# Kernel tuning notes

Measured on AMD Instinct MI355X. Metric: run time of the kernel, lower is better.

The kernel has to match this reference:

```python
import jax, jax.numpy as jnp
import numpy as np

NHEAD = 16  # n_head; head_size N = C // NHEAD = 64


def _forward(x, time_maa_x, time_maa, time_maa_w1, time_maa_w2,
             time_decay, time_decay_w1, time_decay_w2,
             time_aaaaa, time_aaa_w1, time_aaa_w2,
             time_kkk_w1, time_kkk_w2,
             gate_w1, gate_w2,
             time_misc_a, ma_w1, ma_w2,
             time_misc_k, mk_w1, mk_w2,
             receptance, key_w, value, output,
             ln_w, ln_b, time_faaaa):
    B, T, C = x.shape
    H, N = NHEAD, C // NHEAD
    # --- fused_time_shift: token shift + 4-way LoRA mixing (rg, wa, k, v) ---
    xprev = jnp.pad(x, ((0, 0), (1, 0), (0, 0)))[:, :T]   # shift right by one token
    xx = xprev - x
    xxx = x + xx * time_maa_x
    mix = jnp.tanh(xxx @ time_maa_w1.T).reshape(B, T, 4, -1)        # (B,T,4,32)
    deltas = jnp.einsum('btfd,fcd->fbtc', mix, time_maa_w2)         # (4,B,T,C)
    xrg, xwa, xk, xv = x[None] + xx[None] * (time_maa + deltas)
    # --- projections + small LoRAs ---
    r = xrg @ receptance.T
    g = jnp.tanh(xrg @ gate_w1.T) @ gate_w2.T                       # gate
    k = xk @ key_w.T
    kk1 = jnp.tanh(xk @ time_kkk_w1.T)
    mk1 = xk @ mk_w1.T
    v = xv @ value.T
    w1 = jnp.tanh(xwa @ time_decay_w1.T)
    a1 = xwa @ time_aaa_w1.T
    ma1 = xwa @ ma_w1.T
    # data-dependent log-decay, clamped <= -0.5 via softplus
    w = -jax.nn.softplus(-(time_decay + w1 @ time_decay_w2.T)) - 0.5
    # removal key kk: per-head L2-normalized
    kk = k + kk1 @ time_kkk_w2.T
    kk = kk.reshape(B, T, H, N)
    kk = kk / jnp.maximum(jnp.linalg.norm(kk, axis=-1, keepdims=True), 1e-12)
    kk = kk.reshape(B, T, C)
    a = jax.nn.sigmoid(time_aaaaa + a1 @ time_aaa_w2.T)
    ma = jax.nn.sigmoid(time_misc_a + ma1 @ ma_w2.T)
    k = k * ma + k * a * (1 - ma)
    mk = jax.nn.sigmoid(time_misc_k + mk1 @ mk_w2.T)
    k = k * jnp.exp(w * mk)
    b = -kk * a
    # --- RWKV-7 linear-attention scan; state S: (B,H,N_value,N_key) ---
    def heads(z):
        return z.reshape(B, T, H, N).transpose(1, 0, 2, 3)          # (T,B,H,N)
    rh, wh, kh, vh, kkh, bh = map(heads, (r, w, k, v, kk, b))

    def step(S, inp):
        r_, w_, k_, v_, kk_, b_ = inp
        sab = jnp.einsum('bhvk,bhk->bhv', S, kk_)                   # S @ kk
        S = (S * jnp.exp(w_)[:, :, None, :]                         # diag decay on key dim
             + sab[..., None] * b_[:, :, None, :]                   # (S kk) b^T  (delta-rule removal)
             + v_[..., None] * k_[:, :, None, :])                   # v k^T
        y = jnp.einsum('bhvk,bhk->bhv', S, r_)
        return S, y

    S0 = jnp.zeros((B, H, N, N), x.dtype)
    _, y = jax.lax.scan(step, S0, (rh, wh, kh, vh, kkh, bh))
    y = y.transpose(1, 0, 2, 3)                                     # (B,T,H,N)
    # --- GroupNorm (H groups, eps=64e-5) + r.k bonus + gate (fused_attn_ln tail) ---
    mu = y.mean(-1, keepdims=True)
    var = ((y - mu) ** 2).mean(-1, keepdims=True)
    yn = (y - mu) / jnp.sqrt(var + 0.00064) * ln_w.reshape(H, N) + ln_b.reshape(H, N)
    r4 = r.reshape(B, T, H, N)
    k4 = k.reshape(B, T, H, N)
    v4 = v.reshape(B, T, H, N)
    bonus = (r4 * k4 * time_faaaa.reshape(H, N)).sum(-1, keepdims=True) * v4
    out = (yn + bonus).reshape(B, T, C) * g
    return out @ output.T


def setup_inputs() -> dict:
    key = jax.random.key(0)
    ks = iter(jax.random.split(key, 40))
    B, T, C = 2, 1024, 1024
    def n(shape, s=1.0):
        return jax.random.normal(next(ks), shape, jnp.float32) * s
    def u(shape, lo, hi):
        return jax.random.uniform(next(ks), shape, jnp.float32, lo, hi)
    d = {}
    d['x'] = n((B, T, C))
    d['time_maa_x'] = u((1, 1, C), 0.0, 1.0)
    d['time_maa'] = u((4, 1, 1, C), 0.0, 1.0)
    d['time_maa_w1'] = n((128, C), 0.02)
    d['time_maa_w2'] = n((4, C, 32), 0.05)
    d['time_decay'] = u((1, 1, C), -6.5, -1.5)
    d['time_decay_w1'] = n((64, C), 0.02)
    d['time_decay_w2'] = n((C, 64), 0.05)
    d['time_aaaaa'] = n((1, 1, C), 0.1)
    d['time_aaa_w1'] = n((16, C), 0.02)
    d['time_aaa_w2'] = n((C, 16), 0.05)
    d['time_kkk_w1'] = n((16, C), 0.02)
    d['time_kkk_w2'] = n((C, 16), 0.05)
    d['gate_w1'] = n((128, C), 0.05)
    d['gate_w2'] = n((C, 128), 0.05)
    d['time_misc_a'] = n((1, 1, C), 0.1)
    d['ma_w1'] = n((16, C), 0.02)
    d['ma_w2'] = n((C, 16), 0.05)
    d['time_misc_k'] = n((1, 1, C), 0.1)
    d['mk_w1'] = n((16, C), 0.02)
    d['mk_w2'] = n((C, 16), 0.05)
    s = 0.5 / C ** 0.5
    d['receptance'] = u((C, C), -s, s)
    d['key_w'] = u((C, C), -0.1 * s, 0.1 * s)
    d['value'] = u((C, C), -s, s)
    d['output'] = n((C, C), 0.02)
    d['ln_w'] = jnp.ones((C,), jnp.float32)
    d['ln_b'] = jnp.zeros((C,), jnp.float32)
    d['time_faaaa'] = n((C,), 0.1)
    return d


def reference(x, time_maa_x, time_maa, time_maa_w1, time_maa_w2,
              time_decay, time_decay_w1, time_decay_w2,
              time_aaaaa, time_aaa_w1, time_aaa_w2,
              time_kkk_w1, time_kkk_w2,
              gate_w1, gate_w2,
              time_misc_a, ma_w1, ma_w2,
              time_misc_k, mk_w1, mk_w2,
              receptance, key_w, value, output,
              ln_w, ln_b, time_faaaa):
    return _forward(x, time_maa_x, time_maa, time_maa_w1, time_maa_w2,
                    time_decay, time_decay_w1, time_decay_w2,
                    time_aaaaa, time_aaa_w1, time_aaa_w2,
                    time_kkk_w1, time_kkk_w2,
                    gate_w1, gate_w2,
                    time_misc_a, ma_w1, ma_w2,
                    time_misc_k, mk_w1, mk_w2,
                    receptance, key_w, value, output,
                    ln_w, ln_b, time_faaaa)
```

## Files before the change

kernel.cpp:

```cpp
#include <hip/hip_runtime.h>
#include <hip/hip_bf16.h>

typedef __hip_bfloat16 bf16;

#define B_ 2
#define T_ 1024
#define C_ 1024
#define H_ 16
#define N_ 64

using short4v = __attribute__((ext_vector_type(4))) short;
using short8 = __attribute__((ext_vector_type(8))) short;
using f32x4 = __attribute__((ext_vector_type(4))) float;

__device__ __forceinline__ float bs2f(short s) {
  return __uint_as_float(((unsigned int)(unsigned short)s) << 16);
}
__device__ __forceinline__ bf16 f2bf(float f) { return __float2bfloat16(f); }
__device__ __forceinline__ short bfbits(float f) {
  bf16 h = __float2bfloat16(f);
  return *reinterpret_cast<short*>(&h);
}
__device__ __forceinline__ float sigmoidf_(float x) { return 1.0f / (1.0f + expf(-x)); }
__device__ __forceinline__ float softplusf_(float x) {
  return fmaxf(x, 0.0f) + log1pf(expf(-fabsf(x)));
}
__device__ __forceinline__ float qsum16(float x) {
  int a = __builtin_amdgcn_update_dpp(0, __float_as_int(x), 0xB1, 0xF, 0xF, true);
  x += __int_as_float(a);
  int b = __builtin_amdgcn_update_dpp(0, __float_as_int(x), 0x4E, 0xF, 0xF, true);
  x += __int_as_float(b);
  int c = __builtin_amdgcn_update_dpp(0, __float_as_int(x), 0x124, 0xF, 0xF, true);
  x += __int_as_float(c);
  int d = __builtin_amdgcn_update_dpp(0, __float_as_int(x), 0x128, 0xF, 0xF, true);
  x += __int_as_float(d);
  return x;
}
__device__ __forceinline__ void qsum16x2(float& x, float& y) {
  int a0 = __builtin_amdgcn_update_dpp(0, __float_as_int(x), 0xB1, 0xF, 0xF, true);
  int b0 = __builtin_amdgcn_update_dpp(0, __float_as_int(y), 0xB1, 0xF, 0xF, true);
  x += __int_as_float(a0); y += __int_as_float(b0);
  int a1 = __builtin_amdgcn_update_dpp(0, __float_as_int(x), 0x4E, 0xF, 0xF, true);
  int b1 = __builtin_amdgcn_update_dpp(0, __float_as_int(y), 0x4E, 0xF, 0xF, true);
  x += __int_as_float(a1); y += __int_as_float(b1);
  int a2 = __builtin_amdgcn_update_dpp(0, __float_as_int(x), 0x124, 0xF, 0xF, true);
  int b2 = __builtin_amdgcn_update_dpp(0, __float_as_int(y), 0x124, 0xF, 0xF, true);
  x += __int_as_float(a2); y += __int_as_float(b2);
  int a3 = __builtin_amdgcn_update_dpp(0, __float_as_int(x), 0x128, 0xF, 0xF, true);
  int b3 = __builtin_amdgcn_update_dpp(0, __float_as_int(y), 0x128, 0xF, 0xF, true);
  x += __int_as_float(a3); y += __int_as_float(b3);
}

__global__ __launch_bounds__(256) void cvt_all_kernel(
    const float* __restrict__ s0, const float* __restrict__ s1,
    const float* __restrict__ s2, const float* __restrict__ s3,
    const float* __restrict__ s4, const float* __restrict__ s5,
    const float* __restrict__ s6,
    bf16* __restrict__ d0, bf16* __restrict__ d1, bf16* __restrict__ d2w,
    bf16* __restrict__ d3, bf16* __restrict__ d4, bf16* __restrict__ d5,
    bf16* __restrict__ d6,
    const float* __restrict__ tkw1, const float* __restrict__ mkw1,
    const float* __restrict__ tdw1, const float* __restrict__ taw1,
    const float* __restrict__ maw1,
    bf16* __restrict__ wsk, bf16* __restrict__ wswa,
    const float* __restrict__ tmw2, const float* __restrict__ tdw2,
    const float* __restrict__ tkw2, const float* __restrict__ taw2,
    const float* __restrict__ maw2, const float* __restrict__ mkw2,
    bf16* __restrict__ tmw2e, bf16* __restrict__ w2e5) {
  long bidx = blockIdx.x;
  const float* s; bf16* d; long off;
  if (bidx < 4480) {
    long i4 = bidx * 256 + threadIdx.x;
    if (i4 < 32768) { s = s0; d = d0; off = i4; }
    else if (i4 < 294912) { s = s1; d = d1; off = i4 - 32768; }
    else if (i4 < 327680) { s = s2; d = d2w; off = i4 - 294912; }
    else if (i4 < 360448) { s = s3; d = d3; off = i4 - 327680; }
    else if (i4 < 622592) { s = s4; d = d4; off = i4 - 360448; }
    else if (i4 < 884736) { s = s5; d = d5; off = i4 - 622592; }
    else { s = s6; d = d6; off = i4 - 884736; }
  } else if (bidx < 4608) {
    long i4 = (bidx - 4480) * 256 + threadIdx.x;
    long so, dof;
    if (i4 < 4096) { s = tkw1; so = i4; d = wsk; dof = i4; }
    else if (i4 < 8192) { s = mkw1; so = i4 - 4096; d = wsk; dof = i4; }
    else if (i4 < 24576) { s = tdw1; so = i4 - 8192; d = wswa; dof = i4 - 8192; }
    else if (i4 < 28672) { s = taw1; so = i4 - 24576; d = wswa; dof = i4 - 8192; }
    else { s = maw1; so = i4 - 28672; d = wswa; dof = i4 - 8192; }
    float4 v = *(const float4*)(s + so * 4);
    d[dof * 4 + 0] = f2bf(v.x); d[dof * 4 + 1] = f2bf(v.y);
    d[dof * 4 + 2] = f2bf(v.z); d[dof * 4 + 3] = f2bf(v.w);
    return;
  } else if (bidx < 5120) {
    long i4 = (bidx - 4608) * 256 + threadIdx.x;
    long n = i4 >> 5;
    int k0 = (int)(i4 & 31) << 2;
    int f = (int)(n >> 10);
    float4 v = {0.f, 0.f, 0.f, 0.f};
    if ((k0 >> 5) == f) v = *(const float4*)(tmw2 + n * 32 + (k0 & 31));
    tmw2e[i4 * 4 + 0] = f2bf(v.x);
    tmw2e[i4 * 4 + 1] = f2bf(v.y);
    tmw2e[i4 * 4 + 2] = f2bf(v.z);
    tmw2e[i4 * 4 + 3] = f2bf(v.w);
    return;
  } else {
    long i4 = (bidx - 5120) * 256 + threadIdx.x;
    long rowi = i4 >> 5;
    int k0 = (int)(i4 & 31) << 2;
    int j = (int)(rowi >> 10);
    int c = (int)(rowi & 1023);
    float4 v = {0.f, 0.f, 0.f, 0.f};
    if (j == 0) { if (k0 < 64) v = *(const float4*)(tdw2 + c * 64 + k0); }
    else if (j == 1) { if (k0 >= 64 && k0 < 80) v = *(const float4*)(taw2 + c * 16 + (k0 - 64)); }
    else if (j == 2) { if (k0 >= 80 && k0 < 96) v = *(const float4*)(maw2 + c * 16 + (k0 - 80)); }
    else if (j == 3) { if (k0 >= 96 && k0 < 112) v = *(const float4*)(tkw2 + c * 16 + (k0 - 96)); }
    else { if (k0 >= 112) v = *(const float4*)(mkw2 + c * 16 + (k0 - 112)); }
    w2e5[i4 * 4 + 0] = f2bf(v.x);
    w2e5[i4 * 4 + 1] = f2bf(v.y);
    w2e5[i4 * 4 + 2] = f2bf(v.z);
    w2e5[i4 * 4 + 3] = f2bf(v.w);
    return;
  }
  float4 v = *(const float4*)(s + off * 4);
// ... 24 lines not shown
  float* Cf = gb.Cf[z];
  bf16* Cb = gb.Cb[z];
  int tid = threadIdx.x;
  int arow = tid >> 1, acol = (tid & 1) << 5;
  int wrow = tid >> 2, wcol = (tid & 3) << 4;
  int wv = tid >> 6, lane = tid & 63;
  int fr = lane & 15, fq = lane >> 4;
  bool wok = (n0 + wrow) < Nz;
  const bf16* Ap = A + (long)(m0 + arow) * K + acol;
  const bf16* Wp = W + (long)(n0 + wrow) * K + wcol;
  short8 zz = {0, 0, 0, 0, 0, 0, 0, 0};
  f32x4 a00 = {0.f, 0.f, 0.f, 0.f};
  f32x4 a01 = a00, a02 = a00, a03 = a00, a10 = a00, a11 = a00, a12 = a00, a13 = a00;
  for (int k0 = 0; k0 < K; k0 += 64) {
    *(short8*)&As[arow][acol] = *(const short8*)(Ap + k0);
    *(short8*)&As[arow][acol + 8] = *(const short8*)(Ap + k0 + 8);
    *(short8*)&As[arow][acol + 16] = *(const short8*)(Ap + k0 + 16);
    *(short8*)&As[arow][acol + 24] = *(const short8*)(Ap + k0 + 24);
    *(short8*)&Ws[wrow][wcol] = wok ? *(const short8*)(Wp + k0) : zz;
    *(short8*)&Ws[wrow][wcol + 8] = wok ? *(const short8*)(Wp + k0 + 8) : zz;
    __syncthreads();
#pragma unroll
    for (int kk = 0; kk < 2; kk++) {
      int ko = (fq << 3) + (kk << 5);
      short8 af0 = *(const short8*)&As[(wv << 5) + fr][ko];
      short8 af1 = *(const short8*)&As[(wv << 5) + 16 + fr][ko];
      short8 b0 = *(const short8*)&Ws[fr][ko];
      short8 b1 = *(const short8*)&Ws[16 + fr][ko];
      short8 b2 = *(const short8*)&Ws[32 + fr][ko];
      short8 b3 = *(const short8*)&Ws[48 + fr][ko];
      a00 = __builtin_amdgcn_mfma_f32_16x16x32_bf16(af0, b0, a00, 0, 0, 0);
      a01 = __builtin_amdgcn_mfma_f32_16x16x32_bf16(af0, b1, a01, 0, 0, 0);
      a02 = __builtin_amdgcn_mfma_f32_16x16x32_bf16(af0, b2, a02, 0, 0, 0);
      a03 = __builtin_amdgcn_mfma_f32_16x16x32_bf16(af0, b3, a03, 0, 0, 0);
      a10 = __builtin_amdgcn_mfma_f32_16x16x32_bf16(af1, b0, a10, 0, 0, 0);
      a11 = __builtin_amdgcn_mfma_f32_16x16x32_bf16(af1, b1, a11, 0, 0, 0);
      a12 = __builtin_amdgcn_mfma_f32_16x16x32_bf16(af1, b2, a12, 0, 0, 0);
      a13 = __builtin_amdgcn_mfma_f32_16x16x32_bf16(af1, b3, a13, 0, 0, 0);
    }
    __syncthreads();
  }
  int ocol = n0 + fr;
  int orow0 = m0 + (wv << 5) + (fq << 2);
#define WRB(accv, mf, nt) { int col = ocol + ((nt) << 4); if (col < Nz) { \
    _Pragma("unroll") for (int r = 0; r < 4; r++) { \
      float vvv = accv[r]; if (col < actN) vvv = tanhf(vvv); \
      long oi = (long)(orow0 + ((mf) << 4) + r) * ldc + coff + col; \
      if (Cb) Cb[oi] = f2bf(vvv); else Cf[oi] = vvv; } } }
  WRB(a00, 0, 0) WRB(a01, 0, 1) WRB(a02, 0, 2) WRB(a03, 0, 3)
  WRB(a10, 1, 0) WRB(a11, 1, 1) WRB(a12, 1, 2) WRB(a13, 1, 3)
#undef WRB
}

__global__ __launch_bounds__(256) void gemm_mix_kernel(
    const float* __restrict__ x, const float* __restrict__ tmx,
    const bf16* __restrict__ W, bf16* __restrict__ Cb) {
  __shared__ __align__(16) bf16 As[128][72];
  __shared__ __align__(16) bf16 Ws[64][72];
  const int K = 1024;
  int n0 = blockIdx.x << 6;
  int m0 = blockIdx.y << 7;
  int tid = threadIdx.x;
  int arow = tid >> 1, acol = (tid & 1) << 5;
  int wrow = tid >> 2, wcol = (tid & 3) << 4;
  int wv = tid >> 6, lane = tid & 63;
  int fr = lane & 15, fq = lane >> 4;
  int grow = m0 + arow;
  int t = grow & (T_ - 1);
  const float* xp = x + (long)grow * C_ + acol;
  const bf16* Wp = W + (long)(n0 + wrow) * K + wcol;
  f32x4 a00 = {0.f, 0.f, 0.f, 0.f};
  f32x4 a01 = a00, a02 = a00, a03 = a00, a10 = a00, a11 = a00, a12 = a00, a13 = a00;
  for (int k0 = 0; k0 < K; k0 += 64) {
#pragma unroll
    for (int jj = 0; jj < 4; jj++) {
      int co = k0 + (jj << 3);
      float4 c0 = *(const float4*)(xp + co);
      float4 c1 = *(const float4*)(xp + co + 4);
      float4 q0 = {0.f, 0.f, 0.f, 0.f}, q1 = q0;
      if (t > 0) {
        q0 = *(const float4*)(xp + co - C_);
        q1 = *(const float4*)(xp + co + 4 - C_);
      }
      float4 m0v = *(const float4*)(tmx + co + acol);
      float4 m1v = *(const float4*)(tmx + co + acol + 4);
      short8 sv;
      sv[0] = bfbits(fmaf(q0.x - c0.x, m0v.x, c0.x));
      sv[1] = bfbits(fmaf(q0.y - c0.y, m0v.y, c0.y));
      sv[2] = bfbits(fmaf(q0.z - c0.z, m0v.z, c0.z));
      sv[3] = bfbits(fmaf(q0.w - c0.w, m0v.w, c0.w));
      sv[4] = bfbits(fmaf(q1.x - c1.x, m1v.x, c1.x));
      sv[5] = bfbits(fmaf(q1.y - c1.y, m1v.y, c1.y));
      sv[6] = bfbits(fmaf(q1.z - c1.z, m1v.z, c1.z));
      sv[7] = bfbits(fmaf(q1.w - c1.w, m1v.w, c1.w));
      *(short8*)&As[arow][acol + (jj << 3)] = sv;
    }
    *(short8*)&Ws[wrow][wcol] = *(const short8*)(Wp + k0);
    *(short8*)&Ws[wrow][wcol + 8] = *(const short8*)(Wp + k0 + 8);
    __syncthreads();
#pragma unroll
    for (int kk = 0; kk < 2; kk++) {
      int ko = (fq << 3) + (kk << 5);
      short8 af0 = *(const short8*)&As[(wv << 5) + fr][ko];
      short8 af1 = *(const short8*)&As[(wv << 5) + 16 + fr][ko];
      short8 b0 = *(const short8*)&Ws[fr][ko];
      short8 b1 = *(const short8*)&Ws[16 + fr][ko];
      short8 b2 = *(const short8*)&Ws[32 + fr][ko];
      short8 b3 = *(const short8*)&Ws[48 + fr][ko];
      a00 = __builtin_amdgcn_mfma_f32_16x16x32_bf16(af0, b0, a00, 0, 0, 0);
      a01 = __builtin_amdgcn_mfma_f32_16x16x32_bf16(af0, b1, a01, 0, 0, 0);
      a02 = __builtin_amdgcn_mfma_f32_16x16x32_bf16(af0, b2, a02, 0, 0, 0);
      a03 = __builtin_amdgcn_mfma_f32_16x16x32_bf16(af0, b3, a03, 0, 0, 0);
      a10 = __builtin_amdgcn_mfma_f32_16x16x32_bf16(af1, b0, a10, 0, 0, 0);
      a11 = __builtin_amdgcn_mfma_f32_16x16x32_bf16(af1, b1, a11, 0, 0, 0);
      a12 = __builtin_amdgcn_mfma_f32_16x16x32_bf16(af1, b2, a12, 0, 0, 0);
      a13 = __builtin_amdgcn_mfma_f32_16x16x32_bf16(af1, b3, a13, 0, 0, 0);
    }
    __syncthreads();
  }
  const int Nz = 128;
  int ocol = n0 + fr;
  int orow0 = m0 + (wv << 5) + (fq << 2);
#define WRM(accv, mf, nt) { int col = ocol + ((nt) << 4); \
    _Pragma("unroll") for (int r = 0; r < 4; r++) { \
      long oi = (long)(orow0 + ((mf) << 4) + r) * Nz + col; \
      Cb[oi] = f2bf(tanhf(accv[r])); } }
  WRM(a00, 0, 0) WRM(a01, 0, 1) WRM(a02, 0, 2) WRM(a03, 0, 3)
  WRM(a10, 1, 0) WRM(a11, 1, 1) WRM(a12, 1, 2) WRM(a13, 1, 3)
#undef WRM
}

__global__ __launch_bounds__(256) void gemm_mixapply_kernel(
    const bf16* __restrict__ A, const bf16* __restrict__ W,
    const float* __restrict__ x, const float* __restrict__ tmaa,
    bf16* __restrict__ xrg, bf16* __restrict__ xwa,
    bf16* __restrict__ xk, bf16* __restrict__ xv) {
  __shared__ __align__(16) bf16 As[128][72];
  __shared__ __align__(16) bf16 Ws[64][72];
  const int K = 128;
  int n0 = blockIdx.x << 6;
  int m0 = blockIdx.y << 7;
  int tid = threadIdx.x;
  int arow = tid >> 1, acol = (tid & 1) << 5;
  int wrow = tid >> 2, wcol = (tid & 3) << 4;
  int wv = tid >> 6, lane = tid & 63;
  int fr = lane & 15, fq = lane >> 4;
  const bf16* Ap = A + (long)(m0 + arow) * K + acol;
  const bf16* Wp = W + (long)(n0 + wrow) * K + wcol;
  f32x4 a00 = {0.f, 0.f, 0.f, 0.f};
  f32x4 a01 = a00, a02 = a00, a03 = a00, a10 = a00, a11 = a00, a12 = a00, a13 = a00;
  for (int k0 = 0; k0 < K; k0 += 64) {
    *(short8*)&As[arow][acol] = *(const short8*)(Ap + k0);
    *(short8*)&As[arow][acol + 8] = *(const short8*)(Ap + k0 + 8);
    *(short8*)&As[arow][acol + 16] = *(const short8*)(Ap + k0 + 16);
    *(short8*)&As[arow][acol + 24] = *(const short8*)(Ap + k0 + 24);
    *(short8*)&Ws[wrow][wcol] = *(const short8*)(Wp + k0);
    *(short8*)&Ws[wrow][wcol + 8] = *(const short8*)(Wp + k0 + 8);
    __syncthreads();
#pragma unroll
    for (int kk = 0; kk < 2; kk++) {
      int ko = (fq << 3) + (kk << 5);
      short8 af0 = *(const short8*)&As[(wv << 5) + fr][ko];
      short8 af1 = *(const short8*)&As[(wv << 5) + 16 + fr][ko];
      short8 b0 = *(const short8*)&Ws[fr][ko];
      short8 b1 = *(const short8*)&Ws[16 + fr][ko];
      short8 b2 = *(const short8*)&Ws[32 + fr][ko];
      short8 b3 = *(const short8*)&Ws[48 + fr][ko];
      a00 = __builtin_amdgcn_mfma_f32_16x16x32_bf16(af0, b0, a00, 0, 0, 0);
      a01 = __builtin_amdgcn_mfma_f32_16x16x32_bf16(af0, b1, a01, 0, 0, 0);
      a02 = __builtin_amdgcn_mfma_f32_16x16x32_bf16(af0, b2, a02, 0, 0, 0);
      a03 = __builtin_amdgcn_mfma_f32_16x16x32_bf16(af0, b3, a03, 0, 0, 0);
      a10 = __builtin_amdgcn_mfma_f32_16x16x32_bf16(af1, b0, a10, 0, 0, 0);
      a11 = __builtin_amdgcn_mfma_f32_16x16x32_bf16(af1, b1, a11, 0, 0, 0);
      a12 = __builtin_amdgcn_mfma_f32_16x16x32_bf16(af1, b2, a12, 0, 0, 0);
      a13 = __builtin_amdgcn_mfma_f32_16x16x32_bf16(af1, b3, a13, 0, 0, 0);
    }
    __syncthreads();
  }
  int f = n0 >> 10;
  int c0 = n0 & 1023;
  bf16* outp = (f == 0) ? xrg : (f == 1) ? xwa : (f == 2) ? xk : xv;
  int ocol = c0 + fr;
  int orow0 = m0 + (wv << 5) + (fq << 2);
#define WRA(accv, mf, nt) { int cc = ocol + ((nt) << 4); \
    float ta = tmaa[(f << 10) + cc]; \
    _Pragma("unroll") for (int r = 0; r < 4; r++) { \
      int row = orow0 + ((mf) << 4) + r; \
      int t = row & (T_ - 1); \
      long xo = (long)row * C_ + cc; \
      float xb = x[xo]; \
      float xq = (t > 0) ? x[xo - C_] : 0.0f; \
      outp[xo] = f2bf(fmaf(xq - xb, ta + accv[r], xb)); } }
  WRA(a00, 0, 0) WRA(a01, 0, 1) WRA(a02, 0, 2) WRA(a03, 0, 3)
  WRA(a10, 1, 0) WRA(a11, 1, 1) WRA(a12, 1, 2) WRA(a13, 1, 3)
#undef WRA
}

__global__ __launch_bounds__(256) void fuse2_kernel(
    const float* __restrict__ kraw, const float* __restrict__ d2,
    const float* __restrict__ tdec, const float* __restrict__ taa,
    const float* __restrict__ tma, const float* __restrict__ tmk,
    float* __restrict__ ew, float* __restrict__ kfin,
    float* __restrict__ kkn, float* __restrict__ bbo) {
  int m = blockIdx.x, tid = threadIdx.x;
  int c4 = tid << 2;
  const float* dp = d2 + (long)m * 5120;
  float4 wd4 = *(const float4*)(dp + c4);
  float4 ad4 = *(const float4*)(dp + 1024 + c4);
  float4 mad4 = *(const float4*)(dp + 2048 + c4);
  float4 kd4 = *(const float4*)(dp + 3072 + c4);
  float4 mkd4 = *(const float4*)(dp + 4096 + c4);
  float4 kraw4 = *(const float4*)(kraw + (long)m * C_ + c4);
  float4 tdec4 = *(const float4*)(tdec + c4);
  float4 taa4 = *(const float4*)(taa + c4);
  float4 tma4 = *(const float4*)(tma + c4);
  float4 tmk4 = *(const float4*)(tmk + c4);
  float wd[4] = {wd4.x, wd4.y, wd4.z, wd4.w};
  float ad[4] = {ad4.x, ad4.y, ad4.z, ad4.w};
  float mad[4] = {mad4.x, mad4.y, mad4.z, mad4.w};
  float kd[4] = {kd4.x, kd4.y, kd4.z, kd4.w};
  float mkd[4] = {mkd4.x, mkd4.y, mkd4.z, mkd4.w};
  float krw[4] = {kraw4.x, kraw4.y, kraw4.z, kraw4.w};
  float td[4] = {tdec4.x, tdec4.y, tdec4.z, tdec4.w};
  float ta[4] = {taa4.x, taa4.y, taa4.z, taa4.w};
  float tm[4] = {tma4.x, tma4.y, tma4.z, tma4.w};
  float tk[4] = {tmk4.x, tmk4.y, tmk4.z, tmk4.w};
  float kkp[4], av[4], wvv[4], kr[4], mkv[4];
  float sumsq = 0.f;
#pragma unroll
  for (int j = 0; j < 4; j++) {
    float w = -softplusf_(-(td[j] + wd[j])) - 0.5f;
    wvv[j] = w;
    float kkpre = krw[j] + kd[j];
    kkp[j] = kkpre;
    sumsq += kkpre * kkpre;
    float a = sigmoidf_(ta[j] + ad[j]);
    av[j] = a;
    float ma = sigmoidf_(tm[j] + mad[j]);
    float mk = sigmoidf_(tk[j] + mkd[j]);
    mkv[j] = mk;
    kr[j] = krw[j] * (ma + a * (1.f - ma));
  }
  sumsq += __shfl_xor(sumsq, 1);
  sumsq += __shfl_xor(sumsq, 2);
  sumsq += __shfl_xor(sumsq, 4);
  sumsq += __shfl_xor(sumsq, 8);
  float rn = 1.0f / fmaxf(sqrtf(sumsq), 1e-12f);
  float4 kknv, bbov, eww, kfv;
  float* kknp = (float*)&kknv;
  float* bbop = (float*)&bbov;
  float* ewp = (float*)&eww;
  float* kfp = (float*)&kfv;
#pragma unroll
  for (int j = 0; j < 4; j++) {
    float kkx = kkp[j] * rn;
    kknp[j] = kkx;
    bbop[j] = -kkx * av[j];
    ewp[j] = expf(wvv[j]);
    kfp[j] = kr[j] * expf(wvv[j] * mkv[j]);
  }
  long off4 = (long)m * C_ + c4;
  *(float4*)(kkn + off4) = kknv;
  *(float4*)(bbo + off4) = bbov;
  *(float4*)(ew + off4) = eww;
  *(float4*)(kfin + off4) = kfv;
}

#define SCHUNK 16
#define NCHUNK (T_ / SCHUNK)
__global__ __launch_bounds__(256, 1) void scan_kernel(
    const float* __restrict__ rB, const float* __restrict__ ewB,
    const float* __restrict__ kB, const float* __restrict__ vB,
    const float* __restrict__ kkB, const float* __restrict__ bbB,
    float* __restrict__ yB) {
  __shared__ __align__(16) float lds[2][6][SCHUNK * 64];
  int bid = blockIdx.x;
  int bh = bid >> 2, rg = bid & 3;
  int b = bh >> 4, h = bh & 15;
  int tid = threadIdx.x;
  int wave = tid >> 6, lane = tid & 63;
  int g = lane >> 4, q = lane & 15;
  int row = (rg << 4) + (wave << 2) + g;
  int kq = q << 2;
  const long base = ((long)b * T_) * C_ + (h << 6);
  const float* s0 = kkB + base;
  const float* s1 = ewB + base;
  const float* s2 = kB + base;
  const float* s3 = bbB + base;
  const float* s4 = rB + base;
  const float* s5 = vB + base;
  int stok = tid >> 4;
  int spc = (tid & 15) << 2;
  int lo = (stok << 6) + spc;
  float4 rb0, rb1, rb2, rb3, rb4, rb5;
  auto loadc = [&](int c) {
    long go = (long)((c << 4) + stok) * C_ + spc;
    rb0 = *(const float4*)(s0 + go);
    rb1 = *(const float4*)(s1 + go);
    rb2 = *(const float4*)(s2 + go);
    rb3 = *(const float4*)(s3 + go);
    rb4 = *(const float4*)(s4 + go);
    rb5 = *(const float4*)(s5 + go);
  };
  auto stage = [&](int buf) {
    *(float4*)&lds[buf][0][lo] = rb0;
    *(float4*)&lds[buf][1][lo] = rb1;
    *(float4*)&lds[buf][2][lo] = rb2;
    *(float4*)&lds[buf][3][lo] = rb3;
    *(float4*)&lds[buf][4][lo] = rb4;
    *(float4*)&lds[buf][5][lo] = rb5;
  };
  float S0 = 0.f, S1 = 0.f, S2 = 0.f, S3 = 0.f;
  float ypv = 0.f;
  float4 Q0kk, Q0ew, Q0k, Q0bb, Q0r; float Q0v;
  float4 Q1kk, Q1ew, Q1k, Q1bb, Q1r; float Q1v;
  float4 Q2kk, Q2ew, Q2k, Q2bb, Q2r; float Q2v;

#define PF(i, tt) { int tb_ = ((tt) << 6); \
    Q##i##kk = *(const float4*)&lds[cur][0][tb_ + kq]; \
    Q##i##ew = *(const float4*)&lds[cur][1][tb_ + kq]; \
    Q##i##k  = *(const float4*)&lds[cur][2][tb_ + kq]; \
    Q##i##bb = *(const float4*)&lds[cur][3][tb_ + kq]; \
    Q##i##r  = *(const float4*)&lds[cur][4][tb_ + kq]; \
    Q##i##v  = lds[cur][5][tb_ + row]; }
#define SBAR __builtin_amdgcn_sched_barrier(0x7)
#define ST(i, gtok, FIRSTT) { \
    float p_ = fmaf(S1, Q##i##kk.y, S0 * Q##i##kk.x) + \
               fmaf(S3, Q##i##kk.w, S2 * Q##i##kk.z); \
    float yo_ = ypv; \
    qsum16x2(p_, yo_); \
    if (q == 0 && !((FIRSTT) && c == 0)) \
      yB[base + (long)((gtok) - 1) * C_ + row] = yo_; \
    float n0 = fmaf(S0, Q##i##ew.x, Q##i##v * Q##i##k.x); \
    float n1 = fmaf(S1, Q##i##ew.y, Q##i##v * Q##i##k.y); \
    float n2 = fmaf(S2, Q##i##ew.z, Q##i##v * Q##i##k.z); \
    float n3 = fmaf(S3, Q##i##ew.w, Q##i##v * Q##i##k.w); \
    S0 = fmaf(p_, Q##i##bb.x, n0); \
    S1 = fmaf(p_, Q##i##bb.y, n1); \
    S2 = fmaf(p_, Q##i##bb.z, n2); \
    S3 = fmaf(p_, Q##i##bb.w, n3); \
    ypv = fmaf(S1, Q##i##r.y, S0 * Q##i##r.x) + \
          fmaf(S3, Q##i##r.w, S2 * Q##i##r.z); }

  loadc(0);
  stage(0);
  loadc(1);
  __syncthreads();
  int cur = 0;
  for (int c = 0; c < NCHUNK; c++) {
    int t0 = c << 4;
    PF(0, 0); PF(1, 1);
    if (c + 1 < NCHUNK) stage(cur ^ 1);
    if (c + 2 < NCHUNK) loadc(c + 2);
    SBAR;
    PF(2, 2);  SBAR; ST(0, t0 + 0, true);
    PF(0, 3);  SBAR; ST(1, t0 + 1, false);
    PF(1, 4);  SBAR; ST(2, t0 + 2, false);
    PF(2, 5);  SBAR; ST(0, t0 + 3, false);
    PF(0, 6);  SBAR; ST(1, t0 + 4, false);
    PF(1, 7);  SBAR; ST(2, t0 + 5, false);
    PF(2, 8);  SBAR; ST(0, t0 + 6, false);
    PF(0, 9);  SBAR; ST(1, t0 + 7, false);
    PF(1, 10); SBAR; ST(2, t0 + 8, false);
    PF(2, 11); SBAR; ST(0, t0 + 9, false);
    PF(0, 12); SBAR; ST(1, t0 + 10, false);
    PF(1, 13); SBAR; ST(2, t0 + 11, false);
    PF(2, 14); SBAR; ST(0, t0 + 12, false);
    PF(0, 15); SBAR; ST(1, t0 + 13, false);
    ST(2, t0 + 14, false);
    ST(0, t0 + 15, false);
    __syncthreads();
    cur ^= 1;
  }
  {
    float yo = qsum16(ypv);
    if (q == 0) yB[base + (long)(T_ - 1) * C_ + row] = yo;
  }
#undef PF
#undef SBAR
#undef ST
}

__global__ __launch_bounds__(256) void gnout_kernel(
    const float* __restrict__ y, const float* __restrict__ r,
    const float* __restrict__ kf, const float* __restrict__ v,
    const float* __restrict__ g,
    const float* __restrict__ lnw, const float* __restrict__ lnb,
    const float* __restrict__ fa, bf16* __restrict__ z) {
  int tid = threadIdx.x;
  int w = tid >> 6, lane = tid & 63;
  int gi = (blockIdx.x << 2) + w;
  int h = gi & 15, mt = gi >> 4;
  long off = (long)mt * C_ + (h << 6) + lane;
  float yv = y[off];
  float s = yv;
  s += __shfl_xor(s, 1); s += __shfl_xor(s, 2); s += __shfl_xor(s, 4);
  s += __shfl_xor(s, 8); s += __shfl_xor(s, 16); s += __shfl_xor(s, 32);
  float mu = s * (1.0f / 64.0f);
  float d = yv - mu;
  float s2 = d * d;
  s2 += __shfl_xor(s2, 1); s2 += __shfl_xor(s2, 2); s2 += __shfl_xor(s2, 4);
  s2 += __shfl_xor(s2, 8); s2 += __shfl_xor(s2, 16); s2 += __shfl_xor(s2, 32);
  float var = s2 * (1.0f / 64.0f);
  int hc = (h << 6) + lane;
  float dot = r[off] * kf[off] * fa[hc];
  dot += __shfl_xor(dot, 1); dot += __shfl_xor(dot, 2); dot += __shfl_xor(dot, 4);
  dot += __shfl_xor(dot, 8); dot += __shfl_xor(dot, 16); dot += __shfl_xor(dot, 32);
  float yn = d * rsqrtf(var + 0.00064f) * lnw[hc] + lnb[hc];
  z[off] = f2bf((yn + dot * v[off]) * g[off]);
}

extern "C" void kernel_launch(void* const* d_in, const int* in_sizes, int n_in,
                              void* d_out, int out_size, void* d_ws, size_t ws_size,
                              hipStream_t stream) {
  const float* x = (const float*)d_in[0];
  const float* tmx = (const float*)d_in[1];
  const float* tmaa = (const float*)d_in[2];
  const float* tmw1 = (const float*)d_in[3];
  const float* tmw2 = (const float*)d_in[4];
  const float* tdec = (const float*)d_in[5];
  const float* tdw1 = (const float*)d_in[6];
  const float* tdw2 = (const float*)d_in[7];
  const float* taa5 = (const float*)d_in[8];
  const float* taw1 = (const float*)d_in[9];
  const float* taw2 = (const float*)d_in[10];
  const float* tkw1 = (const float*)d_in[11];
  const float* tkw2 = (const float*)d_in[12];
  const float* gw1 = (const float*)d_in[13];
  const float* gw2 = (const float*)d_in[14];
  const float* tmia = (const float*)d_in[15];
  const float* maw1 = (const float*)d_in[16];
  const float* maw2 = (const float*)d_in[17];
  const float* tmik = (const float*)d_in[18];
  const float* mkw1 = (const float*)d_in[19];
  const float* mkw2 = (const float*)d_in[20];
  const float* wrec = (const float*)d_in[21];
  const float* wkey = (const float*)d_in[22];
  const float* wval = (const float*)d_in[23];
  const float* wout = (const float*)d_in[24];
  const float* lnw = (const float*)d_in[25];
  const float* lnb = (const float*)d_in[26];
  const float* faaa = (const float*)d_in[27];

  const long MT = 2048, CC = 1024;
  char* base = (char*)d_ws;
  float* y = (float*)base;     base += MT * CC * 4;
  bf16* xrgb = (bf16*)base;    base += MT * CC * 2;
  bf16* xwab = (bf16*)base;    base += MT * CC * 2;
  bf16* xkb = (bf16*)base;     base += MT * CC * 2;
  bf16* xvb = (bf16*)base;     base += MT * CC * 2;
  float* rr = (float*)base;    base += MT * CC * 4;
  float* kraw = (float*)base;  base += MT * CC * 4;
  float* vv = (float*)base;    base += MT * CC * 4;
  float* gg = (float*)base;    base += MT * CC * 4;
  float* bbo = (float*)base;   base += MT * CC * 4;
  bf16* g1b = (bf16*)base;     base += MT * 128 * 2;
  bf16* out12b = (bf16*)base;  base += MT * 128 * 2;
  bf16* zb = (bf16*)base;      base += MT * CC * 2;
  bf16* mixb = (bf16*)base;    base += MT * 128 * 2;
  float* d2 = (float*)base;    base += MT * 5120L * 4;
  bf16* tmw1b = (bf16*)base;   base += 128 * CC * 2;
  bf16* wrecb = (bf16*)base;   base += CC * CC * 2;
  bf16* gw1b = (bf16*)base;    base += 128 * CC * 2;
  bf16* gw2b = (bf16*)base;    base += CC * 128 * 2;
  bf16* wkeyb = (bf16*)base;   base += CC * CC * 2;
  bf16* wvalb = (bf16*)base;   base += CC * CC * 2;
  bf16* woutb = (bf16*)base;   base += CC * CC * 2;
  bf16* wskb = (bf16*)base;    base += 32 * CC * 2;
  bf16* wswab = (bf16*)base;   base += 96 * CC * 2;
  bf16* tmw2e = (bf16*)base;   base += 4096L * 128 * 2;
  bf16* w2e5b = (bf16*)base;   base += 5120L * 128 * 2;
  float* ew = kraw;
  float* kfin = (float*)xrgb;
  float* kkn = (float*)xkb;

  cvt_all_kernel<<<5760, 256, 0, stream>>>(
      tmw1, wrec, gw1, gw2, wkey, wval, wout,
      tmw1b, wrecb, gw1b, gw2b, wkeyb, wvalb, woutb,
      tkw1, mkw1, tdw1, taw1, maw1, wskb, wswab,
      tmw2, tdw2, tkw2, taw2, maw2, mkw2,
      tmw2e, w2e5b);

  gemm_mix_kernel<<<dim3(2, 16), 256, 0, stream>>>(x, tmx, tmw1b, mixb);
  gemm_mixapply_kernel<<<dim3(64, 16), 256, 0, stream>>>(
      mixb, tmw2e, x, tmaa, xrgb, xwab, xkb, xvb);
  {
    GemmBatch gb = {};
    gb.A[0] = xrgb; gb.W[0] = wrecb; gb.Cf[0] = rr;      gb.Cb[0] = nullptr; gb.N[0] = 1024; gb.actN[0] = 0;   gb.ldc[0] = 1024; gb.coff[0] = 0;
    gb.A[1] = xrgb; gb.W[1] = gw1b;  gb.Cf[1] = nullptr; gb.Cb[1] = g1b;     gb.N[1] = 128;  gb.actN[1] = 128; gb.ldc[1] = 128;  gb.coff[1] = 0;
    gb.A[2] = xkb;  gb.W[2] = wkeyb; gb.Cf[2] = kraw;    gb.Cb[2] = nullptr; gb.N[2] = 1024; gb.actN[2] = 0;   gb.ldc[2] = 1024; gb.coff[2] = 0;
    gb.A[3] = xkb;  gb.W[3] = wskb;  gb.Cf[3] = nullptr; gb.Cb[3] = out12b;  gb.N[3] = 32;   gb.actN[3] = 16;  gb.ldc[3] = 128;  gb.coff[3] = 96;
    gb.A[4] = xvb;  gb.W[4] = wvalb; gb.Cf[4] = vv;      gb.Cb[4] = nullptr; gb.N[4] = 1024; gb.actN[4] = 0;   gb.ldc[4] = 1024; gb.coff[4] = 0;
    gb.A[5] = xwab; gb.W[5] = wswab; gb.Cf[5] = nullptr; gb.Cb[5] = out12b;  gb.N[5] = 96;   gb.actN[5] = 64;  gb.ldc[5] = 128;  gb.coff[5] = 0;
    gemm_batch_kernel<<<dim3(16, 16, 6), 256, 0, stream>>>(gb, 1024);
  }
  {
    GemmBatch gb = {};
    gb.A[0] = g1b;    gb.W[0] = gw2b;  gb.Cf[0] = gg; gb.Cb[0] = nullptr; gb.N[0] = 1024; gb.actN[0] = 0; gb.ldc[0] = 1024; gb.coff[0] = 0;
    gb.A[1] = out12b; gb.W[1] = w2e5b; gb.Cf[1] = d2; gb.Cb[1] = nullptr; gb.N[1] = 5120; gb.actN[1] = 0; gb.ldc[1] = 5120; gb.coff[1] = 0;
    gemm_batch_kernel<<<dim3(80, 16, 2), 256, 0, stream>>>(gb, 128);
  }
  fuse2_kernel<<<2048, 256, 0, stream>>>(kraw, d2, tdec, taa5, tmia, tmik,
                                         ew, kfin, kkn, bbo);
  scan_kernel<<<128, 256, 0, stream>>>(rr, ew, kfin, vv, kkn, bbo, y);
  gnout_kernel<<<8192, 256, 0, stream>>>(y, rr, kfin, vv, gg, lnw, lnb, faaa, zb);
  {
    GemmBatch gb = {};
    gb.A[0] = zb; gb.W[0] = woutb; gb.Cf[0] = (float*)d_out; gb.Cb[0] = nullptr;
    gb.N[0] = 1024; gb.actN[0] = 0; gb.ldc[0] = 1024; gb.coff[0] = 0;
    gemm_batch_kernel<<<dim3(16, 16, 1), 256, 0, stream>>>(gb, 1024);
  }
}
```

Baseline: 429.5 us.

## Fuse mix GEMM into weight-convert kernel and fold elementwise prep into scan

The first mixing GEMM now runs as extra blocks of the weight-conversion kernel, reading fp32 weights and converting them to bf16 on the fly, which removes one launch. The fuse2 elementwise kernel is removed. Its decay, sigmoid, softplus and L2-normalization math now runs inside the scan's chunk staging, reading raw k and the LoRA outputs directly and writing kfin for the later kernel. This cuts two kernel launches and several full-size intermediate round trips through memory. In exchange, the scan, which runs on only 128 blocks, takes on more loads and transcendental work per chunk, and that work may lengthen its serial critical path.

```diff
diff --git a/kernel.cpp b/kernel.cpp
--- a/kernel.cpp
+++ b/kernel.cpp
@@ -51,7 +51,7 @@
   x += __int_as_float(a3); y += __int_as_float(b3);
 }
 
-__global__ __launch_bounds__(256) void cvt_all_kernel(
+__global__ __launch_bounds__(256) void cvt_mix_kernel(
     const float* __restrict__ s0, const float* __restrict__ s1,
     const float* __restrict__ s2, const float* __restrict__ s3,
     const float* __restrict__ s4, const float* __restrict__ s5,
@@ -66,8 +66,98 @@
     const float* __restrict__ tmw2, const float* __restrict__ tdw2,
     const float* __restrict__ tkw2, const float* __restrict__ taw2,
     const float* __restrict__ maw2, const float* __restrict__ mkw2,
-    bf16* __restrict__ tmw2e, bf16* __restrict__ w2e5) {
+    bf16* __restrict__ tmw2e, bf16* __restrict__ w2e5,
+    const float* __restrict__ x, const float* __restrict__ tmx,
+    bf16* __restrict__ mixb) {
   long bidx = blockIdx.x;
+  if (bidx >= 5760) {
+    __shared__ __align__(16) bf16 As[128][72];
+    __shared__ __align__(16) bf16 Ws[64][72];
+    const int K = 1024;
+    int mb = (int)(bidx - 5760);
+    int n0 = (mb & 1) << 6;
+    int m0 = (mb >> 1) << 7;
+    int tid = threadIdx.x;
+    int arow = tid >> 1, acol = (tid & 1) << 5;
+    int wrow = tid >> 2, wcol = (tid & 3) << 4;
+    int wv = tid >> 6, lane = tid & 63;
+    int fr = lane & 15, fq = lane >> 4;
+    int grow = m0 + arow;
+    int t = grow & (T_ - 1);
+    const float* xp = x + (long)grow * C_ + acol;
+    const float* Wp = s0 + (long)(n0 + wrow) * K + wcol;
+    f32x4 a00 = {0.f, 0.f, 0.f, 0.f};
+    f32x4 a01 = a00, a02 = a00, a03 = a00, a10 = a00, a11 = a00, a12 = a00, a13 = a00;
+    for (int k0 = 0; k0 < K; k0 += 64) {
+#pragma unroll
+      for (int jj = 0; jj < 4; jj++) {
+        int co = k0 + (jj << 3);
+        float4 c0 = *(const float4*)(xp + co);
+        float4 c1 = *(const float4*)(xp + co + 4);
+        float4 q0 = {0.f, 0.f, 0.f, 0.f}, q1 = q0;
+        if (t > 0) {
+          q0 = *(const float4*)(xp + co - C_);
+          q1 = *(const float4*)(xp + co + 4 - C_);
+        }
+        float4 m0v = *(const float4*)(tmx + co + acol);
+        float4 m1v = *(const float4*)(tmx + co + acol + 4);
+        short8 sv;
+        sv[0] = bfbits(fmaf(q0.x - c0.x, m0v.x, c0.x));
+        sv[1] = bfbits(fmaf(q0.y - c0.y, m0v.y, c0.y));
+        sv[2] = bfbits(fmaf(q0.z - c0.z, m0v.z, c0.z));
+        sv[3] = bfbits(fmaf(q0.w - c0.w, m0v.w, c0.w));
+        sv[4] = bfbits(fmaf(q1.x - c1.x, m1v.x, c1.x));
+        sv[5] = bfbits(fmaf(q1.y - c1.y, m1v.y, c1.y));
+        sv[6] = bfbits(fmaf(q1.z - c1.z, m1v.z, c1.z));
+        sv[7] = bfbits(fmaf(q1.w - c1.w, m1v.w, c1.w));
+        *(short8*)&As[arow][acol + (jj << 3)] = sv;
+      }
+      {
+        float4 w0 = *(const float4*)(Wp + k0);
+        float4 w1 = *(const float4*)(Wp + k0 + 4);
+        float4 w2 = *(const float4*)(Wp + k0 + 8);
+        float4 w3 = *(const float4*)(Wp + k0 + 12);
+        short8 wv0, wv1;
+        wv0[0] = bfbits(w0.x); wv0[1] = bfbits(w0.y); wv0[2] = bfbits(w0.z); wv0[3] = bfbits(w0.w);
+        wv0[4] = bfbits(w1.x); wv0[5] = bfbits(w1.y); wv0[6] = bfbits(w1.z); wv0[7] = bfbits(w1.w);
+        wv1[0] = bfbits(w2.x); wv1[1] = bfbits(w2.y); wv1[2] = bfbits(w2.z); wv1[3] = bfbits(w2.w);
+        wv1[4] = bfbits(w3.x); wv1[5] = bfbits(w3.y); wv1[6] = bfbits(w3.z); wv1[7] = bfbits(w3.w);
+        *(short8*)&Ws[wrow][wcol] = wv0;
+        *(short8*)&Ws[wrow][wcol + 8] = wv1;
+      }
+      __syncthreads();
+#pragma unroll
+      for (int kk = 0; kk < 2; kk++) {
+        int ko = (fq << 3) + (kk << 5);
+        short8 af0 = *(const short8*)&As[(wv << 5) + fr][ko];
+        short8 af1 = *(const short8*)&As[(wv << 5) + 16 + fr][ko];
+        short8 b0 = *(const short8*)&Ws[fr][ko];
+        short8 b1 = *(const short8*)&Ws[16 + fr][ko];
+        short8 b2 = *(const short8*)&Ws[32 + fr][ko];
+        short8 b3 = *(const short8*)&Ws[48 + fr][ko];
+        a00 = __builtin_amdgcn_mfma_f32_16x16x32_bf16(af0, b0, a00, 0, 0, 0);
+        a01 = __builtin_amdgcn_mfma_f32_16x16x32_bf16(af0, b1, a01, 0, 0, 0);
+        a02 = __builtin_amdgcn_mfma_f32_16x16x32_bf16(af0, b2, a02, 0, 0, 0);
+        a03 = __builtin_amdgcn_mfma_f32_16x16x32_bf16(af0, b3, a03, 0, 0, 0);
+        a10 = __builtin_amdgcn_mfma_f32_16x16x32_bf16(af1, b0, a10, 0, 0, 0);
+        a11 = __builtin_amdgcn_mfma_f32_16x16x32_bf16(af1, b1, a11, 0, 0, 0);
+        a12 = __builtin_amdgcn_mfma_f32_16x16x32_bf16(af1, b2, a12, 0, 0, 0);
+        a13 = __builtin_amdgcn_mfma_f32_16x16x32_bf16(af1, b3, a13, 0, 0, 0);
+      }
+      __syncthreads();
+    }
+    const int Nz = 128;
+    int ocol = n0 + fr;
+    int orow0 = m0 + (wv << 5) + (fq << 2);
+#define WRM(accv, mf, nt) { int col = ocol + ((nt) << 4); \
+    _Pragma("unroll") for (int r = 0; r < 4; r++) { \
+      long oi = (long)(orow0 + ((mf) << 4) + r) * Nz + col; \
+      mixb[oi] = f2bf(tanhf(accv[r])); } }
+    WRM(a00, 0, 0) WRM(a01, 0, 1) WRM(a02, 0, 2) WRM(a03, 0, 3)
+    WRM(a10, 1, 0) WRM(a11, 1, 1) WRM(a12, 1, 2) WRM(a13, 1, 3)
+#undef WRM
+    return;
+  }
   const float* s; bf16* d; long off;
   if (bidx < 4480) {
     long i4 = bidx * 256 + threadIdx.x;
@@ -198,84 +288,6 @@
 #undef WRB
 }
 
-__global__ __launch_bounds__(256) void gemm_mix_kernel(
-    const float* __restrict__ x, const float* __restrict__ tmx,
-    const bf16* __restrict__ W, bf16* __restrict__ Cb) {
-  __shared__ __align__(16) bf16 As[128][72];
-  __shared__ __align__(16) bf16 Ws[64][72];
-  const int K = 1024;
-  int n0 = blockIdx.x << 6;
-  int m0 = blockIdx.y << 7;
-  int tid = threadIdx.x;
-  int arow = tid >> 1, acol = (tid & 1) << 5;
-  int wrow = tid >> 2, wcol = (tid & 3) << 4;
-  int wv = tid >> 6, lane = tid & 63;
-  int fr = lane & 15, fq = lane >> 4;
-  int grow = m0 + arow;
-  int t = grow & (T_ - 1);
-  const float* xp = x + (long)grow * C_ + acol;
-  const bf16* Wp = W + (long)(n0 + wrow) * K + wcol;
-  f32x4 a00 = {0.f, 0.f, 0.f, 0.f};
-  f32x4 a01 = a00, a02 = a00, a03 = a00, a10 = a00, a11 = a00, a12 = a00, a13 = a00;
-  for (int k0 = 0; k0 < K; k0 += 64) {
-#pragma unroll
-    for (int jj = 0; jj < 4; jj++) {
-      int co = k0 + (jj << 3);
-      float4 c0 = *(const float4*)(xp + co);
-      float4 c1 = *(const float4*)(xp + co + 4);
-      float4 q0 = {0.f, 0.f, 0.f, 0.f}, q1 = q0;
-      if (t > 0) {
-        q0 = *(const float4*)(xp + co - C_);
-        q1 = *(const float4*)(xp + co + 4 - C_);
-      }
-      float4 m0v = *(const float4*)(tmx + co + acol);
-      float4 m1v = *(const float4*)(tmx + co + acol + 4);
-      short8 sv;
-      sv[0] = bfbits(fmaf(q0.x - c0.x, m0v.x, c0.x));
-      sv[1] = bfbits(fmaf(q0.y - c0.y, m0v.y, c0.y));
-      sv[2] = bfbits(fmaf(q0.z - c0.z, m0v.z, c0.z));
-      sv[3] = bfbits(fmaf(q0.w - c0.w, m0v.w, c0.w));
-      sv[4] = bfbits(fmaf(q1.x - c1.x, m1v.x, c1.x));
-      sv[5] = bfbits(fmaf(q1.y - c1.y, m1v.y, c1.y));
-      sv[6] = bfbits(fmaf(q1.z - c1.z, m1v.z, c1.z));
-      sv[7] = bfbits(fmaf(q1.w - c1.w, m1v.w, c1.w));
-      *(short8*)&As[arow][acol + (jj << 3)] = sv;
-    }
-    *(short8*)&Ws[wrow][wcol] = *(const short8*)(Wp + k0);
-    *(short8*)&Ws[wrow][wcol + 8] = *(const short8*)(Wp + k0 + 8);
-    __syncthreads();
-#pragma unroll
-    for (int kk = 0; kk < 2; kk++) {
-      int ko = (fq << 3) + (kk << 5);
-      short8 af0 = *(const short8*)&As[(wv << 5) + fr][ko];
-      short8 af1 = *(const short8*)&As[(wv << 5) + 16 + fr][ko];
-      short8 b0 = *(const short8*)&Ws[fr][ko];
-      short8 b1 = *(const short8*)&Ws[16 + fr][ko];
-      short8 b2 = *(const short8*)&Ws[32 + fr][ko];
-      short8 b3 = *(const short8*)&Ws[48 + fr][ko];
-      a00 = __builtin_amdgcn_mfma_f32_16x16x32_bf16(af0, b0, a00, 0, 0, 0);
-      a01 = __builtin_amdgcn_mfma_f32_16x16x32_bf16(af0, b1, a01, 0, 0, 0);
-      a02 = __builtin_amdgcn_mfma_f32_16x16x32_bf16(af0, b2, a02, 0, 0, 0);
-      a03 = __builtin_amdgcn_mfma_f32_16x16x32_bf16(af0, b3, a03, 0, 0, 0);
-      a10 = __builtin_amdgcn_mfma_f32_16x16x32_bf16(af1, b0, a10, 0, 0, 0);
-      a11 = __builtin_amdgcn_mfma_f32_16x16x32_bf16(af1, b1, a11, 0, 0, 0);
-      a12 = __builtin_amdgcn_mfma_f32_16x16x32_bf16(af1, b2, a12, 0, 0, 0);
-      a13 = __builtin_amdgcn_mfma_f32_16x16x32_bf16(af1, b3, a13, 0, 0, 0);
-    }
-    __syncthreads();
-  }
-  const int Nz = 128;
-  int ocol = n0 + fr;
-  int orow0 = m0 + (wv << 5) + (fq << 2);
-#define WRM(accv, mf, nt) { int col = ocol + ((nt) << 4); \
-    _Pragma("unroll") for (int r = 0; r < 4; r++) { \
-      long oi = (long)(orow0 + ((mf) << 4) + r) * Nz + col; \
-      Cb[oi] = f2bf(tanhf(accv[r])); } }
-  WRM(a00, 0, 0) WRM(a01, 0, 1) WRM(a02, 0, 2) WRM(a03, 0, 3)
-  WRM(a10, 1, 0) WRM(a11, 1, 1) WRM(a12, 1, 2) WRM(a13, 1, 3)
-#undef WRM
-}
-
 __global__ __launch_bounds__(256) void gemm_mixapply_kernel(
     const bf16* __restrict__ A, const bf16* __restrict__ W,
     const float* __restrict__ x, const float* __restrict__ tmaa,
@@ -342,83 +354,14 @@
 #undef WRA
 }
 
-__global__ __launch_bounds__(256) void fuse2_kernel(
-    const float* __restrict__ kraw, const float* __restrict__ d2,
-    const float* __restrict__ tdec, const float* __restrict__ taa,
-    const float* __restrict__ tma, const float* __restrict__ tmk,
-    float* __restrict__ ew, float* __restrict__ kfin,
-    float* __restrict__ kkn, float* __restrict__ bbo) {
-  int m = blockIdx.x, tid = threadIdx.x;
-  int c4 = tid << 2;
-  const float* dp = d2 + (long)m * 5120;
-  float4 wd4 = *(const float4*)(dp + c4);
-  float4 ad4 = *(const float4*)(dp + 1024 + c4);
-  float4 mad4 = *(const float4*)(dp + 2048 + c4);
-  float4 kd4 = *(const float4*)(dp + 3072 + c4);
-  float4 mkd4 = *(const float4*)(dp + 4096 + c4);
-  float4 kraw4 = *(const float4*)(kraw + (long)m * C_ + c4);
-  float4 tdec4 = *(const float4*)(tdec + c4);
-  float4 taa4 = *(const float4*)(taa + c4);
-  float4 tma4 = *(const float4*)(tma + c4);
-  float4 tmk4 = *(const float4*)(tmk + c4);
-  float wd[4] = {wd4.x, wd4.y, wd4.z, wd4.w};
-  float ad[4] = {ad4.x, ad4.y, ad4.z, ad4.w};
-  float mad[4] = {mad4.x, mad4.y, mad4.z, mad4.w};
-  float kd[4] = {kd4.x, kd4.y, kd4.z, kd4.w};
-  float mkd[4] = {mkd4.x, mkd4.y, mkd4.z, mkd4.w};
-  float krw[4] = {kraw4.x, kraw4.y, kraw4.z, kraw4.w};
-  float td[4] = {tdec4.x, tdec4.y, tdec4.z, tdec4.w};
-  float ta[4] = {taa4.x, taa4.y, taa4.z, taa4.w};
-  float tm[4] = {tma4.x, tma4.y, tma4.z, tma4.w};
-  float tk[4] = {tmk4.x, tmk4.y, tmk4.z, tmk4.w};
-  float kkp[4], av[4], wvv[4], kr[4], mkv[4];
-  float sumsq = 0.f;
-#pragma unroll
-  for (int j = 0; j < 4; j++) {
-    float w = -softplusf_(-(td[j] + wd[j])) - 0.5f;
-    wvv[j] = w;
-    float kkpre = krw[j] + kd[j];
-    kkp[j] = kkpre;
-    sumsq += kkpre * kkpre;
-    float a = sigmoidf_(ta[j] + ad[j]);
-    av[j] = a;
-    float ma = sigmoidf_(tm[j] + mad[j]);
-    float mk = sigmoidf_(tk[j] + mkd[j]);
-    mkv[j] = mk;
-    kr[j] = krw[j] * (ma + a * (1.f - ma));
-  }
-  sumsq += __shfl_xor(sumsq, 1);
-  sumsq += __shfl_xor(sumsq, 2);
-  sumsq += __shfl_xor(sumsq, 4);
-  sumsq += __shfl_xor(sumsq, 8);
-  float rn = 1.0f / fmaxf(sqrtf(sumsq), 1e-12f);
-  float4 kknv, bbov, eww, kfv;
-  float* kknp = (float*)&kknv;
-  float* bbop = (float*)&bbov;
-  float* ewp = (float*)&eww;
-  float* kfp = (float*)&kfv;
-#pragma unroll
-  for (int j = 0; j < 4; j++) {
-    float kkx = kkp[j] * rn;
-    kknp[j] = kkx;
-    bbop[j] = -kkx * av[j];
-    ewp[j] = expf(wvv[j]);
-    kfp[j] = kr[j] * expf(wvv[j] * mkv[j]);
-  }
-  long off4 = (long)m * C_ + c4;
-  *(float4*)(kkn + off4) = kknv;
-  *(float4*)(bbo + off4) = bbov;
-  *(float4*)(ew + off4) = eww;
-  *(float4*)(kfin + off4) = kfv;
-}
-
 #define SCHUNK 16
 #define NCHUNK (T_ / SCHUNK)
 __global__ __launch_bounds__(256, 1) void scan_kernel(
-    const float* __restrict__ rB, const float* __restrict__ ewB,
-    const float* __restrict__ kB, const float* __restrict__ vB,
-    const float* __restrict__ kkB, const float* __restrict__ bbB,
-    float* __restrict__ yB) {
+    const float* __restrict__ rB, const float* __restrict__ vvB,
+    const float* __restrict__ krawB, const float* __restrict__ d2B,
+    const float* __restrict__ tdec, const float* __restrict__ taa,
+    const float* __restrict__ tma, const float* __restrict__ tmk,
+    float* __restrict__ yB, float* __restrict__ kfB) {
   __shared__ __align__(16) float lds[2][6][SCHUNK * 64];
   int bid = blockIdx.x;
   int bh = bid >> 2, rg = bid & 3;
@@ -429,32 +372,62 @@
   int row = (rg << 4) + (wave << 2) + g;
   int kq = q << 2;
   const long base = ((long)b * T_) * C_ + (h << 6);
-  const float* s0 = kkB + base;
-  const float* s1 = ewB + base;
-  const float* s2 = kB + base;
-  const float* s3 = bbB + base;
-  const float* s4 = rB + base;
-  const float* s5 = vB + base;
+  const float* sR = rB + base;
+  const float* sV = vvB + base;
+  const float* sKr = krawB + base;
   int stok = tid >> 4;
   int spc = (tid & 15) << 2;
   int lo = (stok << 6) + spc;
-  float4 rb0, rb1, rb2, rb3, rb4, rb5;
+  int ch = (h << 6) + spc;
+  float4 td4 = *(const float4*)(tdec + ch);
+  float4 ta4 = *(const float4*)(taa + ch);
+  float4 tm4 = *(const float4*)(tma + ch);
+  float4 tk4 = *(const float4*)(tmk + ch);
+  float4 rbR, rbV, rbKr, rbWd, rbAd, rbMad, rbKd, rbMkd;
   auto loadc = [&](int c) {
-    long go = (long)((c << 4) + stok) * C_ + spc;
-    rb0 = *(const float4*)(s0 + go);
-    rb1 = *(const float4*)(s1 + go);
-    rb2 = *(const float4*)(s2 + go);
-    rb3 = *(const float4*)(s3 + go);
-    rb4 = *(const float4*)(s4 + go);
-    rb5 = *(const float4*)(s5 + go);
+    int m = (c << 4) + stok;
+    long gr = (long)m * C_ + spc;
+    rbR = *(const float4*)(sR + gr);
+    rbV = *(const float4*)(sV + gr);
+    rbKr = *(const float4*)(sKr + gr);
+    long gd = (long)(b * T_ + m) * 5120 + ch;
+    rbWd = *(const float4*)(d2B + gd);
+    rbAd = *(const float4*)(d2B + gd + 1024);
+    rbMad = *(const float4*)(d2B + gd + 2048);
+    rbKd = *(const float4*)(d2B + gd + 3072);
+    rbMkd = *(const float4*)(d2B + gd + 4096);
   };
-  auto stage = [&](int buf) {
-    *(float4*)&lds[buf][0][lo] = rb0;
-    *(float4*)&lds[buf][1][lo] = rb1;
-    *(float4*)&lds[buf][2][lo] = rb2;
-    *(float4*)&lds[buf][3][lo] = rb3;
-    *(float4*)&lds[buf][4][lo] = rb4;
-    *(float4*)&lds[buf][5][lo] = rb5;
+  auto stage = [&](int buf, int cc) {
+    float kk0 = rbKr.x + rbKd.x, kk1 = rbKr.y + rbKd.y;
+    float kk2 = rbKr.z + rbKd.z, kk3 = rbKr.w + rbKd.w;
+    float ss = fmaf(kk0, kk0, fmaf(kk1, kk1, fmaf(kk2, kk2, kk3 * kk3)));
+    ss = qsum16(ss);
+    float rn = 1.0f / fmaxf(sqrtf(ss), 1e-12f);
+    float w0 = -softplusf_(-(td4.x + rbWd.x)) - 0.5f;
+    float w1 = -softplusf_(-(td4.y + rbWd.y)) - 0.5f;
+    float w2 = -softplusf_(-(td4.z + rbWd.z)) - 0.5f;
+    float w3 = -softplusf_(-(td4.w + rbWd.w)) - 0.5f;
+    float a0 = sigmoidf_(ta4.x + rbAd.x), a1 = sigmoidf_(ta4.y + rbAd.y);
+    float a2 = sigmoidf_(ta4.z + rbAd.z), a3 = sigmoidf_(ta4.w + rbAd.w);
+    float p0 = sigmoidf_(tm4.x + rbMad.x), p1 = sigmoidf_(tm4.y + rbMad.y);
+    float p2 = sigmoidf_(tm4.z + rbMad.z), p3 = sigmoidf_(tm4.w + rbMad.w);
+    float k0 = sigmoidf_(tk4.x + rbMkd.x), k1 = sigmoidf_(tk4.y + rbMkd.y);
+    float k2 = sigmoidf_(tk4.z + rbMkd.z), k3 = sigmoidf_(tk4.w + rbMkd.w);
+    float4 eww = {expf(w0), expf(w1), expf(w2), expf(w3)};
+    float4 kfv;
+    kfv.x = rbKr.x * (p0 + a0 * (1.f - p0)) * expf(w0 * k0);
+    kfv.y = rbKr.y * (p1 + a1 * (1.f - p1)) * expf(w1 * k1);
+    kfv.z = rbKr.z * (p2 + a2 * (1.f - p2)) * expf(w2 * k2);
+    kfv.w = rbKr.w * (p3 + a3 * (1.f - p3)) * expf(w3 * k3);
+    float4 kknv = {kk0 * rn, kk1 * rn, kk2 * rn, kk3 * rn};
+    float4 bbv = {-kknv.x * a0, -kknv.y * a1, -kknv.z * a2, -kknv.w * a3};
+    *(float4*)&lds[buf][0][lo] = kknv;
+    *(float4*)&lds[buf][1][lo] = eww;
+    *(float4*)&lds[buf][2][lo] = kfv;
+    *(float4*)&lds[buf][3][lo] = bbv;
+    *(float4*)&lds[buf][4][lo] = rbR;
+    *(float4*)&lds[buf][5][lo] = rbV;
+    *(float4*)(kfB + base + (long)((cc << 4) + stok) * C_ + spc) = kfv;
   };
   float S0 = 0.f, S1 = 0.f, S2 = 0.f, S3 = 0.f;
   float ypv = 0.f;
@@ -489,14 +462,14 @@
           fmaf(S3, Q##i##r.w, S2 * Q##i##r.z); }
 
   loadc(0);
-  stage(0);
+  stage(0, 0);
   loadc(1);
   __syncthreads();
   int cur = 0;
   for (int c = 0; c < NCHUNK; c++) {
     int t0 = c << 4;
     PF(0, 0); PF(1, 1);
-    if (c + 1 < NCHUNK) stage(cur ^ 1);
+    if (c + 1 < NCHUNK) stage(cur ^ 1, c + 1);
     if (c + 2 < NCHUNK) loadc(c + 2);
     SBAR;
     PF(2, 2);  SBAR; ST(0, t0 + 0, true);
@@ -599,7 +572,6 @@
   float* kraw = (float*)base;  base += MT * CC * 4;
   float* vv = (float*)base;    base += MT * CC * 4;
   float* gg = (float*)base;    base += MT * CC * 4;
-  float* bbo = (float*)base;   base += MT * CC * 4;
   bf16* g1b = (bf16*)base;     base += MT * 128 * 2;
   bf16* out12b = (bf16*)base;  base += MT * 128 * 2;
   bf16* zb = (bf16*)base;      base += MT * CC * 2;
@@ -616,18 +588,15 @@
   bf16* wswab = (bf16*)base;   base += 96 * CC * 2;
   bf16* tmw2e = (bf16*)base;   base += 4096L * 128 * 2;
   bf16* w2e5b = (bf16*)base;   base += 5120L * 128 * 2;
-  float* ew = kraw;
   float* kfin = (float*)xrgb;
-  float* kkn = (float*)xkb;
-
-  cvt_all_kernel<<<5760, 256, 0, stream>>>(
+
+  cvt_mix_kernel<<<5792, 256, 0, stream>>>(
       tmw1, wrec, gw1, gw2, wkey, wval, wout,
       tmw1b, wrecb, gw1b, gw2b, wkeyb, wvalb, woutb,
       tkw1, mkw1, tdw1, taw1, maw1, wskb, wswab,
       tmw2, tdw2, tkw2, taw2, maw2, mkw2,
-      tmw2e, w2e5b);
-
-  gemm_mix_kernel<<<dim3(2, 16), 256, 0, stream>>>(x, tmx, tmw1b, mixb);
+      tmw2e, w2e5b, x, tmx, mixb);
+
   gemm_mixapply_kernel<<<dim3(64, 16), 256, 0, stream>>>(
       mixb, tmw2e, x, tmaa, xrgb, xwab, xkb, xvb);
   {
@@ -646,9 +615,8 @@
     gb.A[1] = out12b; gb.W[1] = w2e5b; gb.Cf[1] = d2; gb.Cb[1] = nullptr; gb.N[1] = 5120; gb.actN[1] = 0; gb.ldc[1] = 5120; gb.coff[1] = 0;
     gemm_batch_kernel<<<dim3(80, 16, 2), 256, 0, stream>>>(gb, 128);
   }
-  fuse2_kernel<<<2048, 256, 0, stream>>>(kraw, d2, tdec, taa5, tmia, tmik,
-                                         ew, kfin, kkn, bbo);
-  scan_kernel<<<128, 256, 0, stream>>>(rr, ew, kfin, vv, kkn, bbo, y);
+  scan_kernel<<<128, 256, 0, stream>>>(rr, vv, kraw, d2,
+                                       tdec, taa5, tmia, tmik, y, kfin);
   gnout_kernel<<<8192, 256, 0, stream>>>(y, rr, kfin, vv, gg, lnw, lnb, faaa, zb);
   {
     GemmBatch gb = {};
```

Measured after the change: 576.8 us. 1.34x slower.
